# Performance work log

Hardware: AMD Instinct MI355X
Metric: run time of the kernel (lower is better)

## Reference

```python
import jax, jax.numpy as jnp
import numpy as np

T, D_IN, N_RES, D_OUT = 16384, 8, 2048, 8
LEAK = 0.9            # leak_rate
SPECTRAL_RADIUS = 0.9
SPARSITY = 0.1
INPUT_SCALING = 1.0
BIAS_SCALING = 0.2


def setup_inputs() -> dict:
    key = jax.random.key(0)
    k1, k2, k3, k4, k5, k6 = jax.random.split(key, 6)
    inputs = jax.random.normal(k1, (T, D_IN), dtype=jnp.float32)
    W_in = INPUT_SCALING * jax.random.normal(k2, (N_RES, D_IN), dtype=jnp.float32)
    # Sparse recurrent matrix scaled to approximate spectral radius.
    mask = (jax.random.uniform(k3, (N_RES, N_RES)) < SPARSITY).astype(jnp.float32)
    W_raw = jax.random.normal(k4, (N_RES, N_RES), dtype=jnp.float32) * mask
    # Gaussian matrix with density p has spectral radius ~ std*sqrt(p*N).
    W = W_raw * (SPECTRAL_RADIUS / np.sqrt(SPARSITY * N_RES))
    b = BIAS_SCALING * jax.random.normal(k5, (N_RES,), dtype=jnp.float32)
    W_out = jax.random.normal(k6, (D_OUT, N_RES + 1), dtype=jnp.float32) / np.sqrt(N_RES)
    return {"inputs": inputs, "W_in": W_in, "W": W, "b": b, "W_out": W_out}


def reference(inputs, W_in, W, b, W_out):
    # Leaky-integrator ESN: x_t = (1-a) x_{t-1} + a tanh(W_in u_t + W x_{t-1} + b)
    # Precompute all input projections (T, N) in one GEMM.
    u_proj = inputs @ W_in.T + b  # (T, N)

    def step(x, up):
        x_new = (1.0 - LEAK) * x + LEAK * jnp.tanh(up + W @ x)
        return x_new, x_new

    x0 = jnp.zeros((W.shape[0],), dtype=inputs.dtype)
    _, xs = jax.lax.scan(step, x0, u_proj)  # xs: (T, N)
    # Readout: y_t = W_out @ [x_t; 1]  (washout = 0, so all T kept)
    Y = xs @ W_out[:, :-1].T + W_out[:, -1]  # (T, D_OUT)
    return Y
```

## Files before the change

### kernel.cpp

```cpp
#include <hip/hip_runtime.h>
#include <math.h>


#define T_STEPS 16384
#define NRES    2048
#define DIN     8
#define DOUT    8
#define NBLK    128
#define NTHR    512
#define ROWS    16
#define LEAK    0.9f
#define OML     0.1f
#define SPIN_LIMIT 150000

typedef unsigned long long u64;

#define AL(p) __hip_atomic_load((p), __ATOMIC_RELAXED, __HIP_MEMORY_SCOPE_AGENT)

__launch_bounds__(NTHR, 1)
__global__ void esn_persistent(const float* __restrict__ inputs,
                               const float* __restrict__ W_in,
                               const float* __restrict__ W,
                               const float* __restrict__ bvec,
                               const float* __restrict__ W_out,
                               float* __restrict__ Y,
                               u64*   __restrict__ xt)
{
    __shared__ float W_lds[ROWS][NRES];
    __shared__ float x_lds[NRES];
    __shared__ float xnew_lds[ROWS];
    __shared__ float xin_lds[DIN];
    __shared__ float Win_lds[ROWS][DIN];
    __shared__ float b_lds[ROWS];

    const int b    = blockIdx.x;
    const int tid  = threadIdx.x;
    const int lid  = tid & 63;
    const int wv   = tid >> 6;
    const int row0 = b * ROWS;

    #pragma unroll
    for (int i = 0; i < ROWS * (NRES / 4) / NTHR; ++i) {
        const int idx = i * NTHR + tid;
        const int r = idx >> 9, c = idx & 511;
        ((float4*)&W_lds[r][0])[c] =
            ((const float4*)(W + (size_t)(row0 + r) * NRES))[c];
    }
    if (tid < ROWS * DIN)
        Win_lds[tid >> 3][tid & 7] = W_in[(row0 + (tid >> 3)) * DIN + (tid & 7)];
    if (tid < ROWS) b_lds[tid] = bvec[row0 + tid];

    float xin_reg = (tid < DIN) ? inputs[tid] : 0.f;

    auto readout = [&](int tp) {
        const float* Wr = W_out + (size_t)wv * (NRES + 1);
        float a = 0.f;
        #pragma unroll
        for (int k = 0; k < NRES / 64; ++k)
            a += Wr[lid + 64 * k] * x_lds[lid + 64 * k];
        #pragma unroll
        for (int off = 32; off; off >>= 1) a += __shfl_xor(a, off);
        if (lid == 0) Y[(size_t)tp * DOUT + wv] = a + Wr[NRES];
    };

    for (int t = 0; ; ++t) {
        int okall = 1;
        if (t > 0) {
            const u64* src = xt + (size_t)((t - 1) & 1) * NRES;
            u64 v0 = 0, v1 = 0, v2 = 0, v3 = 0;
            int ok0 = 0, ok1 = 0, ok2 = 0, ok3 = 0;
            for (int it = 0; !(ok0 & ok1 & ok2 & ok3) && it < SPIN_LIMIT; ++it) {
                if (!ok0) { v0 = AL(src + tid);            ok0 = ((int)(v0 >> 32) == t); }
                if (!ok1) { v1 = AL(src + tid + NTHR);     ok1 = ((int)(v1 >> 32) == t); }
                if (!ok2) { v2 = AL(src + tid + 2 * NTHR); ok2 = ((int)(v2 >> 32) == t); }
                if (!ok3) { v3 = AL(src + tid + 3 * NTHR); ok3 = ((int)(v3 >> 32) == t); }
            }
            x_lds[tid]            = __uint_as_float((unsigned)v0);
            x_lds[tid + NTHR]     = __uint_as_float((unsigned)v1);
            x_lds[tid + 2 * NTHR] = __uint_as_float((unsigned)v2);
            x_lds[tid + 3 * NTHR] = __uint_as_float((unsigned)v3);
            okall = ok0 & ok1 & ok2 & ok3;
        } else {
            ((float4*)x_lds)[tid] = make_float4(0.f, 0.f, 0.f, 0.f);
        }
        if (t < T_STEPS && tid < DIN) xin_lds[tid] = xin_reg;

        if (!__syncthreads_and(okall)) break;

        if (t == T_STEPS) {
            if (b == ((t - 1) & (NBLK - 1))) readout(t - 1);
            break;
        }

        const int r0 = wv * 2, r1 = r0 + 1;
        float acc0 = 0.f, acc1 = 0.f;
        #pragma unroll
        for (int k = 0; k < NRES / 64; ++k) {
            const float xv = x_lds[lid + 64 * k];
            acc0 += W_lds[r0][lid + 64 * k] * xv;
            acc1 += W_lds[r1][lid + 64 * k] * xv;
        }
        #pragma unroll
        for (int off = 32; off; off >>= 1) {
            acc0 += __shfl_xor(acc0, off);
            acc1 += __shfl_xor(acc1, off);
        }
        if (lid == 0 || lid == 32) {
            const int   rl = (lid == 0) ? r0 : r1;
            const float s  = (lid == 0) ? acc0 : acc1;
            float u = b_lds[rl];
            #pragma unroll
            for (int j = 0; j < DIN; ++j) u += Win_lds[rl][j] * xin_lds[j];
            xnew_lds[rl] = OML * x_lds[row0 + rl] + LEAK * tanhf(u + s);
        }
        __syncthreads();

        if (wv == 0 && lid < ROWS) {
            const u64 rec = ((u64)(unsigned)(t + 1) << 32)
                          | (u64)__float_as_uint(xnew_lds[lid]);
            __hip_atomic_store(xt + (size_t)(t & 1) * NRES + row0 + lid, rec,
                               __ATOMIC_RELAXED, __HIP_MEMORY_SCOPE_AGENT);
        }

        if (tid < DIN && t + 1 < T_STEPS)
            xin_reg = inputs[(size_t)(t + 1) * DIN + tid];
        if (t > 0 && b == ((t - 1) & (NBLK - 1))) readout(t - 1);
    }
}

extern "C" void kernel_launch(void* const* d_in, const int* in_sizes, int n_in,
                              void* d_out, int out_size, void* d_ws, size_t ws_size,
                              hipStream_t stream) {
    const float* inputs = (const float*)d_in[0];
    const float* W_in   = (const float*)d_in[1];
    const float* W      = (const float*)d_in[2];
    const float* bvec   = (const float*)d_in[3];
    const float* W_out  = (const float*)d_in[4];
    float* Y = (float*)d_out;

    u64* xt = (u64*)d_ws;

    esn_persistent<<<NBLK, NTHR, 0, stream>>>(inputs, W_in, W, bvec, W_out,
                                              Y, xt);
}
```

Baseline: 56.20 ms.

## Double-buffer state in LDS and drop per-step barrier before publishing

Double-buffers the x and input-vector LDS arrays by step parity so the next step's writes cannot race with reads from the current step. This removes the second __syncthreads per timestep and the xnew staging array. Each owning lane now publishes its tagged state value to global memory straight after its reduction. The goal is a shorter critical path per recurrent step in the persistent, spin-synchronized kernel, paid for with extra LDS and reliance on the parity buffering for correctness.

```diff
diff --git a/kernel.cpp b/kernel.cpp
--- a/kernel.cpp
+++ b/kernel.cpp
@@ -27,9 +27,8 @@
                                u64*   __restrict__ xt)
 {
     __shared__ float W_lds[ROWS][NRES];
-    __shared__ float x_lds[NRES];
-    __shared__ float xnew_lds[ROWS];
-    __shared__ float xin_lds[DIN];
+    __shared__ float x_lds[2][NRES];
+    __shared__ float xin_lds[2][DIN];
     __shared__ float Win_lds[ROWS][DIN];
     __shared__ float b_lds[ROWS];
 
@@ -52,18 +51,21 @@
 
     float xin_reg = (tid < DIN) ? inputs[tid] : 0.f;
 
-    auto readout = [&](int tp) {
+    auto readout = [&](int tp, const float* xb) {
         const float* Wr = W_out + (size_t)wv * (NRES + 1);
         float a = 0.f;
         #pragma unroll
         for (int k = 0; k < NRES / 64; ++k)
-            a += Wr[lid + 64 * k] * x_lds[lid + 64 * k];
+            a += Wr[lid + 64 * k] * xb[lid + 64 * k];
         #pragma unroll
         for (int off = 32; off; off >>= 1) a += __shfl_xor(a, off);
         if (lid == 0) Y[(size_t)tp * DOUT + wv] = a + Wr[NRES];
     };
 
     for (int t = 0; ; ++t) {
+        const int p = (t + 1) & 1;
+        float* xb = &x_lds[p][0];
+
         int okall = 1;
         if (t > 0) {
             const u64* src = xt + (size_t)((t - 1) & 1) * NRES;
@@ -75,20 +77,20 @@
                 if (!ok2) { v2 = AL(src + tid + 2 * NTHR); ok2 = ((int)(v2 >> 32) == t); }
                 if (!ok3) { v3 = AL(src + tid + 3 * NTHR); ok3 = ((int)(v3 >> 32) == t); }
             }
-            x_lds[tid]            = __uint_as_float((unsigned)v0);
-            x_lds[tid + NTHR]     = __uint_as_float((unsigned)v1);
-            x_lds[tid + 2 * NTHR] = __uint_as_float((unsigned)v2);
-            x_lds[tid + 3 * NTHR] = __uint_as_float((unsigned)v3);
+            xb[tid]            = __uint_as_float((unsigned)v0);
+            xb[tid + NTHR]     = __uint_as_float((unsigned)v1);
+            xb[tid + 2 * NTHR] = __uint_as_float((unsigned)v2);
+            xb[tid + 3 * NTHR] = __uint_as_float((unsigned)v3);
             okall = ok0 & ok1 & ok2 & ok3;
         } else {
-            ((float4*)x_lds)[tid] = make_float4(0.f, 0.f, 0.f, 0.f);
+            ((float4*)xb)[tid] = make_float4(0.f, 0.f, 0.f, 0.f);
         }
-        if (t < T_STEPS && tid < DIN) xin_lds[tid] = xin_reg;
+        if (t < T_STEPS && tid < DIN) xin_lds[p][tid] = xin_reg;
 
         if (!__syncthreads_and(okall)) break;
 
         if (t == T_STEPS) {
-            if (b == ((t - 1) & (NBLK - 1))) readout(t - 1);
+            if (b == ((t - 1) & (NBLK - 1))) readout(t - 1, xb);
             break;
         }
 
@@ -96,7 +98,7 @@
         float acc0 = 0.f, acc1 = 0.f;
         #pragma unroll
         for (int k = 0; k < NRES / 64; ++k) {
-            const float xv = x_lds[lid + 64 * k];
+            const float xv = xb[lid + 64 * k];
             acc0 += W_lds[r0][lid + 64 * k] * xv;
             acc1 += W_lds[r1][lid + 64 * k] * xv;
         }
@@ -105,26 +107,23 @@
             acc0 += __shfl_xor(acc0, off);
             acc1 += __shfl_xor(acc1, off);
         }
+
         if (lid == 0 || lid == 32) {
             const int   rl = (lid == 0) ? r0 : r1;
             const float s  = (lid == 0) ? acc0 : acc1;
             float u = b_lds[rl];
             #pragma unroll
-            for (int j = 0; j < DIN; ++j) u += Win_lds[rl][j] * xin_lds[j];
-            xnew_lds[rl] = OML * x_lds[row0 + rl] + LEAK * tanhf(u + s);
-        }
-        __syncthreads();
-
-        if (wv == 0 && lid < ROWS) {
+            for (int j = 0; j < DIN; ++j) u += Win_lds[rl][j] * xin_lds[p][j];
+            const float xn = OML * xb[row0 + rl] + LEAK * tanhf(u + s);
             const u64 rec = ((u64)(unsigned)(t + 1) << 32)
-                          | (u64)__float_as_uint(xnew_lds[lid]);
-            __hip_atomic_store(xt + (size_t)(t & 1) * NRES + row0 + lid, rec,
+                          | (u64)__float_as_uint(xn);
+            __hip_atomic_store(xt + (size_t)(t & 1) * NRES + row0 + rl, rec,
                                __ATOMIC_RELAXED, __HIP_MEMORY_SCOPE_AGENT);
         }
 
         if (tid < DIN && t + 1 < T_STEPS)
             xin_reg = inputs[(size_t)(t + 1) * DIN + tid];
-        if (t > 0 && b == ((t - 1) & (NBLK - 1))) readout(t - 1);
+        if (t > 0 && b == ((t - 1) & (NBLK - 1))) readout(t - 1, xb);
     }
 }
 
```

Result: no change. 55.77 ms (-0.8%).
